# Kernel tuning notes

Hardware: AMD Instinct MI355X
Metric: run time of the kernel (lower is better)

The kernel has to match this reference:

```python
import jax, jax.numpy as jnp
import numpy as np

N = 100000
E = 1600000
IN_C, HID, OUT_C = 512, 256, 32
K = 10
ALPHA = 0.1


def setup_inputs() -> dict:
    key = jax.random.key(0)
    ks = jax.random.split(key, 8)
    x = jax.random.normal(ks[0], (N, IN_C), dtype=jnp.float32)
    edge_index = jax.random.randint(ks[1], (2, E), 0, N, dtype=jnp.int64)
    def lin(k, fan_in, fan_out):
        kw, kb = jax.random.split(k)
        bound = 1.0 / np.sqrt(fan_in)
        W = jax.random.uniform(kw, (fan_out, fan_in), minval=-bound, maxval=bound, dtype=jnp.float32)
        b = jax.random.uniform(kb, (fan_out,), minval=-bound, maxval=bound, dtype=jnp.float32)
        return W, b
    W1, b1 = lin(ks[2], IN_C, HID)
    Wr, br = lin(ks[3], HID, HID)
    W2, b2 = lin(ks[4], HID, OUT_C)
    return {"x": x, "edge_index": edge_index, "W1": W1, "b1": b1,
            "Wr": Wr, "br": br, "W2": W2, "b2": b2}


def _appnp(h0, row, col, norm):
    # h = (1-alpha) * A_hat h + alpha * h0, K steps
    def step(h, _):
        msg = norm[:, None] * h[row]                      # [E+N, C] gather
        agg = jax.ops.segment_sum(msg, col, num_segments=N)
        return (1.0 - ALPHA) * agg + ALPHA * h0, None
    h, _ = jax.lax.scan(step, h0, None, length=K)
    return h


def reference(x, edge_index, W1, b1, Wr, br, W2, b2):
    # eval mode: dropout p=0 -> identity
    h1 = jax.nn.relu(x @ W1.T + b1)
    h2 = jax.nn.relu(h1 @ Wr.T + br)
    x_res = h1 + h2
    h0 = x_res @ W2.T + b2                                # [N, OUT_C]

    # gcn_norm with self-loops (PyG default for APPNP)
    loops = jnp.arange(N, dtype=edge_index.dtype)
    row = jnp.concatenate([edge_index[0], loops])
    col = jnp.concatenate([edge_index[1], loops])
    deg = jax.ops.segment_sum(jnp.ones_like(col, dtype=h0.dtype), col, num_segments=N)
    dinv = jnp.where(deg > 0, jax.lax.rsqrt(deg), 0.0)
    norm = dinv[row] * dinv[col]                          # [E+N]

    return _appnp(h0, row, col, norm)
```

## Files before the change

kernel.cpp:

```cpp
#include <hip/hip_runtime.h>

#define N_NODES 100000
#define E_EDGES 1600000
#define IN_CH   512
#define HID     256
#define OUT_CH  32
#define K_STEPS 10

typedef unsigned short u16;
typedef unsigned int   u32;

typedef __attribute__((ext_vector_type(8))) short bf16x8;
typedef __attribute__((ext_vector_type(4))) float f32x4;

__device__ __forceinline__ float b2f(u16 u) {
    union { u32 i; float f; } x; x.i = ((u32)u) << 16; return x.f;
}
__device__ __forceinline__ u16 f2b(float f) {
    union { float f; u32 u; } x; x.f = f;
    u32 r = x.u + 0x7fffu + ((x.u >> 16) & 1u);
    return (u16)(r >> 16);
}

__device__ __forceinline__ void load_lds16(const void* g, void* l) {
    __builtin_amdgcn_global_load_lds(
        (const __attribute__((address_space(1))) unsigned int*)g,
        (__attribute__((address_space(3))) unsigned int*)l,
        16, 0, 0);
}


__global__ __launch_bounds__(256) void k_cast(const float* __restrict__ in, u16* __restrict__ out, int n4) {
    int i = blockIdx.x * 256 + threadIdx.x;
    if (i < n4) {
        float4 f = ((const float4*)in)[i];
        ushort4 u;
        u.x = f2b(f.x); u.y = f2b(f.y); u.z = f2b(f.z); u.w = f2b(f.w);
        ((ushort4*)out)[i] = u;
    }
}


__global__ __launch_bounds__(256) void k_count(const int* __restrict__ col, int* __restrict__ cnt) {
    int i = blockIdx.x * 256 + threadIdx.x;
    if (i < E_EDGES) atomicAdd(&cnt[col[i]], 1);
}

__global__ __launch_bounds__(256) void k_dinv(const int* __restrict__ cnt, float* __restrict__ dinv) {
    int i = blockIdx.x * 256 + threadIdx.x;
    if (i < N_NODES) dinv[i] = rsqrtf((float)(cnt[i] + 1));
}

__global__ __launch_bounds__(256) void k_blocksum(const int* __restrict__ cnt, int* __restrict__ bs) {
    int b = blockIdx.x, t = threadIdx.x;
    int idx = b * 1024 + t * 4;
    int s = 0;
    #pragma unroll
    for (int j = 0; j < 4; ++j) if (idx + j < N_NODES) s += cnt[idx + j];
    #pragma unroll
    for (int d = 32; d > 0; d >>= 1) s += __shfl_down(s, d, 64);
    __shared__ int smem[4];
    int lane = t & 63, w = t >> 6;
    if (lane == 0) smem[w] = s;
    __syncthreads();
    if (t == 0) bs[b] = smem[0] + smem[1] + smem[2] + smem[3];
}

__global__ void k_scanblocks(const int* __restrict__ bs, int* __restrict__ bo, int nb) {
    int t = threadIdx.x;
    int v = (t < nb) ? bs[t] : 0;
    int incl = v;
    int lane = t & 63, w = t >> 6;
    #pragma unroll
    for (int d = 1; d < 64; d <<= 1) { int tt = __shfl_up(incl, d, 64); if (lane >= d) incl += tt; }
    __shared__ int wsum[2];
    if (lane == 63) wsum[w] = incl;
    __syncthreads();
    int add = (w == 1) ? wsum[0] : 0;
    if (t < nb) bo[t] = add + incl - v;
}

__global__ __launch_bounds__(256) void k_scanwithin(const int* __restrict__ cnt, const int* __restrict__ bo,
                                                    int* __restrict__ off) {
    int b = blockIdx.x, t = threadIdx.x;
    int idx = b * 1024 + t * 4;
    int v[4]; int s = 0;
    #pragma unroll
    for (int j = 0; j < 4; ++j) { v[j] = (idx + j < N_NODES) ? cnt[idx + j] : 0; s += v[j]; }
    int incl = s;
    int lane = t & 63, w = t >> 6;
    #pragma unroll
    for (int d = 1; d < 64; d <<= 1) { int tt = __shfl_up(incl, d, 64); if (lane >= d) incl += tt; }
    __shared__ int wsum[4];
    if (lane == 63) wsum[w] = incl;
    __syncthreads();
    int woff = 0;
    #pragma unroll
    for (int k = 0; k < 4; ++k) if (k < w) woff += wsum[k];
    int run = bo[b] + woff + incl - s;
    #pragma unroll
    for (int j = 0; j < 4; ++j) { if (idx + j < N_NODES) off[idx + j] = run; run += v[j]; }
    if (b == 0 && t == 0) off[N_NODES] = E_EDGES;
}

__global__ __launch_bounds__(256) void k_fill(const int* __restrict__ row, const int* __restrict__ col,
                                              const int* __restrict__ off, int* __restrict__ cursor,
                                              int* __restrict__ csr_row) {
    int i = blockIdx.x * 256 + threadIdx.x;
    if (i < E_EDGES) {
        int c = col[i];
        int pos = off[c] + atomicAdd(&cursor[c], 1);
        csr_row[pos] = row[i];
    }
}


template<int KDIM, bool RESID, bool AF32>
__global__ __launch_bounds__(256) void gemm_mfma(const void* __restrict__ Aptr,
                                                 const u16* __restrict__ Bt,
                                                 const float* __restrict__ bias,
                                                 const u16* __restrict__ resid,
                                                 u16* __restrict__ Out,
                                                 int M) {
    __shared__ u16 As[128 * 32];
    __shared__ u16 Bs[128 * 32];
    const int t = threadIdx.x;
    const int lane = t & 63, w = t >> 6;
    const int row0 = blockIdx.x * 128, col0 = blockIdx.y * 128;

    f32x4 acc[4][4] = {};

    const int rr = lane >> 2;
    const int cc = lane & 3;

    const int wr = (w >> 1) * 64, wc = (w & 1) * 64;
    const int fr = lane & 15, quad = lane >> 4;

    for (int k0 = 0; k0 < KDIM; k0 += 32) {
        if constexpr (AF32) {
            const float* A = (const float*)Aptr;
            #pragma unroll
            for (int it = 0; it < 4; ++it) {
                int chunk = it * 256 + t;
                int row = chunk >> 3, seg = chunk & 7;
                int gr = row0 + row;
                if (gr > M - 1) gr = M - 1;
                float4 f = *(const float4*)&A[(size_t)gr * KDIM + k0 + seg * 4];
                u32 lo = (u32)f2b(f.x) | ((u32)f2b(f.y) << 16);
                u32 hi = (u32)f2b(f.z) | ((u32)f2b(f.w) << 16);
                *(uint2*)&As[row * 32 + seg * 4] = make_uint2(lo, hi);
            }
        } else {
            const u16* A = (const u16*)Aptr;
            #pragma unroll
            for (int rep = 0; rep < 2; ++rep) {
                int ii = w * 2 + rep;
                int gr = row0 + ii * 16 + rr;
                if (gr > M - 1) gr = M - 1;
                load_lds16(A + (size_t)gr * KDIM + k0 + cc * 8, &As[ii * 512]);
            }
        }
        #pragma unroll
        for (int rep = 0; rep < 2; ++rep) {
            int ii = w * 2 + rep;
            int gc = col0 + ii * 16 + rr;
            load_lds16(Bt + (size_t)gc * KDIM + k0 + cc * 8, &Bs[ii * 512]);
        }
        __syncthreads();

        bf16x8 af[4], bfr[4];
        #pragma unroll
        for (int ti = 0; ti < 4; ++ti)
            af[ti] = *(const bf16x8*)&As[(wr + ti * 16 + fr) * 32 + quad * 8];
        #pragma unroll
        for (int tj = 0; tj < 4; ++tj)
            bfr[tj] = *(const bf16x8*)&Bs[(wc + tj * 16 + fr) * 32 + quad * 8];
        #pragma unroll
        for (int ti = 0; ti < 4; ++ti)
            #pragma unroll
            for (int tj = 0; tj < 4; ++tj)
                acc[ti][tj] = __builtin_amdgcn_mfma_f32_16x16x32_bf16(af[ti], bfr[tj], acc[ti][tj], 0, 0, 0);
        __syncthreads();
    }

    #pragma unroll
    for (int tj = 0; tj < 4; ++tj) {
        int col = col0 + wc + tj * 16 + fr;
        float bv = bias[col];
        #pragma unroll
        for (int ti = 0; ti < 4; ++ti) {
            #pragma unroll
            for (int r = 0; r < 4; ++r) {
                int grow = row0 + wr + ti * 16 + quad * 4 + r;
                if (grow < M) {
                    float v = fmaxf(acc[ti][tj][r] + bv, 0.f);
                    if constexpr (RESID) v += b2f(resid[(size_t)grow * HID + col]);
                    Out[(size_t)grow * HID + col] = f2b(v);
                }
            }
        }
    }
}

__global__ __launch_bounds__(256) void gemm_out(const u16* __restrict__ xres, const float* __restrict__ W2,
                                                const float* __restrict__ b2, const float* __restrict__ dinv,
                                                float* __restrict__ h0, u16* __restrict__ p0, int M) {
    constexpr int BM = 128, BK = 16, KDIM = HID;
    __shared__ float As[BK][BM + 4];
    __shared__ float Bs[BK][OUT_CH + 4];
    int t = threadIdx.x;
    int row0 = blockIdx.x * BM;

    float acc[4][4];
    #pragma unroll
    for (int i = 0; i < 4; ++i)
        #pragma unroll
        for (int j = 0; j < 4; ++j) acc[i][j] = 0.f;

    for (int k0 = 0; k0 < KDIM; k0 += BK) {
        #pragma unroll
        for (int rep = 0; rep < 2; ++rep) {
            int idx = rep * 256 + t;
            int r = idx >> 2, ch = idx & 3;
            int gr = row0 + r;
            float v0, v1, v2, v3;
            if (gr < M) {
                ushort4 u = *(const ushort4*)&xres[(size_t)gr * KDIM + k0 + ch * 4];
                v0 = b2f(u.x); v1 = b2f(u.y); v2 = b2f(u.z); v3 = b2f(u.w);
            } else { v0 = v1 = v2 = v3 = 0.f; }
            As[ch * 4 + 0][r] = v0; As[ch * 4 + 1][r] = v1;
            As[ch * 4 + 2][r] = v2; As[ch * 4 + 3][r] = v3;
        }
        if (t < 128) {
            int nn = t >> 2, ch = t & 3;
            float4 f = *(const float4*)&W2[(size_t)nn * KDIM + k0 + ch * 4];
            Bs[ch * 4 + 0][nn] = f.x; Bs[ch * 4 + 1][nn] = f.y;
            Bs[ch * 4 + 2][nn] = f.z; Bs[ch * 4 + 3][nn] = f.w;
        }
        __syncthreads();
        int ty = t >> 3, tx = t & 7;
        #pragma unroll
        for (int kk = 0; kk < BK; ++kk) {
            float a[4], wv[4];
            *(float4*)&a[0] = *(const float4*)&As[kk][ty * 4];
            *(float4*)&wv[0] = *(const float4*)&Bs[kk][tx * 4];
            #pragma unroll
            for (int i = 0; i < 4; ++i)
                #pragma unroll
                for (int j = 0; j < 4; ++j) acc[i][j] = fmaf(a[i], wv[j], acc[i][j]);
        }
        __syncthreads();
    }
    int ty = t >> 3, tx = t & 7;
    #pragma unroll
    for (int i = 0; i < 4; ++i) {
        int gr = row0 + ty * 4 + i;
        if (gr < M) {
            float dv = dinv[gr];
            float4 v;
            v.x = acc[i][0] + b2[tx * 4 + 0];
            v.y = acc[i][1] + b2[tx * 4 + 1];
            v.z = acc[i][2] + b2[tx * 4 + 2];
            v.w = acc[i][3] + b2[tx * 4 + 3];
            *(float4*)&h0[(size_t)gr * OUT_CH + tx * 4] = v;
            ushort4 u;
            u.x = f2b(dv * v.x); u.y = f2b(dv * v.y);
            u.z = f2b(dv * v.z); u.w = f2b(dv * v.w);
            *(ushort4*)&p0[(size_t)gr * OUT_CH + tx * 4] = u;
        }
    }
}


__global__ __launch_bounds__(256) void k_prop(const u32* __restrict__ pin, u32* __restrict__ pout,
                                              float* __restrict__ hout, const float* __restrict__ h0,
                                              const int* __restrict__ off, const int* __restrict__ csr_row,
                                              const float* __restrict__ dinv, int last) {
    int t = threadIdx.x;
    int gw = blockIdx.x * 16 + (t >> 4);
    int l = t & 15;
    int lbase = t & 48;
    int s = off[gw], e = off[gw + 1];
    float dv = dinv[gw];
    u32 selfp = pin[(size_t)gw * 16 + l];
    float2 h0v = ((const float2*)h0)[(size_t)gw * 16 + l];

    float acc0 = 0.f, acc1 = 0.f;
    for (int base = s; base < e; base += 16) {
        int n = e - base; if (n > 16) n = 16;
        int idx = (base + l < e) ? csr_row[base + l] : 0;
        int i = 0;
        for (; i + 3 < n; i += 4) {
            int r0 = __shfl(idx, lbase + i + 0, 64);
            int r1 = __shfl(idx, lbase + i + 1, 64);
            int r2 = __shfl(idx, lbase + i + 2, 64);
            int r3 = __shfl(idx, lbase + i + 3, 64);
            u32 v0 = pin[(size_t)r0 * 16 + l];
            u32 v1 = pin[(size_t)r1 * 16 + l];
            u32 v2 = pin[(size_t)r2 * 16 + l];
            u32 v3 = pin[(size_t)r3 * 16 + l];
            acc0 += (b2f((u16)v0) + b2f((u16)v1)) + (b2f((u16)v2) + b2f((u16)v3));
            acc1 += (b2f((u16)(v0 >> 16)) + b2f((u16)(v1 >> 16))) +
                    (b2f((u16)(v2 >> 16)) + b2f((u16)(v3 >> 16)));
        }
        for (; i < n; ++i) {
            int r = __shfl(idx, lbase + i, 64);
            u32 v = pin[(size_t)r * 16 + l];
            acc0 += b2f((u16)v);
            acc1 += b2f((u16)(v >> 16));
        }
    }
    acc0 += b2f((u16)selfp);
    acc1 += b2f((u16)(selfp >> 16));
    float hc0 = 0.9f * dv * acc0 + 0.1f * h0v.x;
    float hc1 = 0.9f * dv * acc1 + 0.1f * h0v.y;
    if (last) {
        ((float2*)hout)[(size_t)gw * 16 + l] = make_float2(hc0, hc1);
    } else {
        pout[(size_t)gw * 16 + l] = (u32)f2b(dv * hc0) | ((u32)f2b(dv * hc1) << 16);
    }
}


extern "C" void kernel_launch(void* const* d_in, const int* in_sizes, int n_in,
                              void* d_out, int out_size, void* d_ws, size_t ws_size,
                              hipStream_t stream) {
    const float* x  = (const float*)d_in[0];
    const int*   ei = (const int*)d_in[1];
    const float* W1 = (const float*)d_in[2];
    const float* b1 = (const float*)d_in[3];
    const float* Wr = (const float*)d_in[4];
    const float* br = (const float*)d_in[5];
    const float* W2 = (const float*)d_in[6];
    const float* b2 = (const float*)d_in[7];
    float* out = (float*)d_out;

    char* ws = (char*)d_ws;
    size_t off_b = 0;
    auto take = [&](size_t bytes) {
        void* p = ws + off_b;
        off_b += (bytes + 255) & ~(size_t)255;
        return p;
    };

    float* h0      = (float*)take((size_t)N_NODES * OUT_CH * 4);
    u16*   pA      = (u16*)  take((size_t)N_NODES * OUT_CH * 2);
    u16*   pB      = (u16*)  take((size_t)N_NODES * OUT_CH * 2);
    int*   csr_row = (int*)  take((size_t)E_EDGES * 4);
    float* dinv    = (float*)take((size_t)N_NODES * 4);
    int*   cnt     = (int*)  take((size_t)N_NODES * 4);
    int*   offs    = (int*)  take((size_t)(N_NODES + 1) * 4);
    int*   cursor  = (int*)  take((size_t)N_NODES * 4);
    int*   bs      = (int*)  take(1024);
    int*   bo      = (int*)  take(1024);
    u16*   h1      = (u16*)  take((size_t)N_NODES * HID * 2);
    u16*   xres    = (u16*)  take((size_t)N_NODES * HID * 2);
    u16*   W1b     = (u16*)  take((size_t)HID * IN_CH * 2);
    u16*   Wrb     = (u16*)  take((size_t)HID * HID * 2);

    const int* e_row = ei;
    const int* e_col = ei + E_EDGES;

    k_cast<<<(HID * IN_CH / 4 + 255) / 256, 256, 0, stream>>>(W1, W1b, HID * IN_CH / 4);
    k_cast<<<(HID * HID / 4 + 255) / 256, 256, 0, stream>>>(Wr, Wrb, HID * HID / 4);

    dim3 g12((N_NODES + 127) / 128, HID / 128);
    gemm_mfma<IN_CH, false, true><<<g12, 256, 0, stream>>>(x, W1b, b1, nullptr, h1, N_NODES);

    hipMemsetAsync(cnt, 0, (size_t)N_NODES * 4, stream);
    hipMemsetAsync(cursor, 0, (size_t)N_NODES * 4, stream);
    const int NB = (N_NODES + 1023) / 1024;
    k_count<<<(E_EDGES + 255) / 256, 256, 0, stream>>>(e_col, cnt);
    k_dinv<<<(N_NODES + 255) / 256, 256, 0, stream>>>(cnt, dinv);
    k_blocksum<<<NB, 256, 0, stream>>>(cnt, bs);
    k_scanblocks<<<1, 128, 0, stream>>>(bs, bo, NB);
    k_scanwithin<<<NB, 256, 0, stream>>>(cnt, bo, offs);
    k_fill<<<(E_EDGES + 255) / 256, 256, 0, stream>>>(e_row, e_col, offs, cursor, csr_row);

    gemm_mfma<HID, true, false><<<g12, 256, 0, stream>>>(h1, Wrb, br, h1, xres, N_NODES);

    gemm_out<<<(N_NODES + 127) / 128, 256, 0, stream>>>(xres, W2, b2, dinv, h0, pA, N_NODES);

    const u32* pin = (const u32*)pA;
    for (int s = 0; s < K_STEPS; ++s) {
        int last = (s == K_STEPS - 1);
        u32* pout = (u32*)((s & 1) ? pA : pB);
        k_prop<<<N_NODES / 16, 256, 0, stream>>>(pin, pout, out, h0, offs, csr_row, dinv, last);
        pin = pout;
    }
}
```

Before: 919.7 us.

## Pad CSR rows to 16 with a dummy zero node and double-buffer the first GEMM

Each node's CSR segment is rounded up to a multiple of 16 and filled with a dummy index that points at an extra all-zero row in the ping-pong buffers. The propagation kernel can then issue 16 unconditional gathers per chunk with no tail loop or bounds checks, which raises memory-level parallelism. The first GEMM is split into its own kernel that double-buffers LDS and prefetches the fp32 A tile into registers, overlapping global loads with MFMA work. In exchange it adds padded CSR storage, wasted gathers of the zero row, and extra setup kernels and memsets.

Measured after the change: 889.0 us. -3.3%, faster.

```diff
diff --git a/kernel.cpp b/kernel.cpp
--- a/kernel.cpp
+++ b/kernel.cpp
@@ -6,6 +6,7 @@
 #define HID     256
 #define OUT_CH  32
 #define K_STEPS 10
+#define EPAD    (E_EDGES + 16 * N_NODES)
 
 typedef unsigned short u16;
 typedef unsigned int   u32;
@@ -51,12 +52,14 @@
     if (i < N_NODES) dinv[i] = rsqrtf((float)(cnt[i] + 1));
 }
 
+__device__ __forceinline__ int pad16(int v) { return (v + 15) & ~15; }
+
 __global__ __launch_bounds__(256) void k_blocksum(const int* __restrict__ cnt, int* __restrict__ bs) {
     int b = blockIdx.x, t = threadIdx.x;
     int idx = b * 1024 + t * 4;
     int s = 0;
     #pragma unroll
-    for (int j = 0; j < 4; ++j) if (idx + j < N_NODES) s += cnt[idx + j];
+    for (int j = 0; j < 4; ++j) if (idx + j < N_NODES) s += pad16(cnt[idx + j]);
     #pragma unroll
     for (int d = 32; d > 0; d >>= 1) s += __shfl_down(s, d, 64);
     __shared__ int smem[4];
@@ -86,7 +89,7 @@
     int idx = b * 1024 + t * 4;
     int v[4]; int s = 0;
     #pragma unroll
-    for (int j = 0; j < 4; ++j) { v[j] = (idx + j < N_NODES) ? cnt[idx + j] : 0; s += v[j]; }
+    for (int j = 0; j < 4; ++j) { v[j] = (idx + j < N_NODES) ? pad16(cnt[idx + j]) : 0; s += v[j]; }
     int incl = s;
     int lane = t & 63, w = t >> 6;
     #pragma unroll
@@ -100,7 +103,16 @@
     int run = bo[b] + woff + incl - s;
     #pragma unroll
     for (int j = 0; j < 4; ++j) { if (idx + j < N_NODES) off[idx + j] = run; run += v[j]; }
-    if (b == 0 && t == 0) off[N_NODES] = E_EDGES;
+}
+
+__global__ __launch_bounds__(256) void k_total(const int* __restrict__ bo, const int* __restrict__ bs,
+                                               int* __restrict__ off, int nb) {
+    off[N_NODES] = bo[nb - 1] + bs[nb - 1];
+}
+
+__global__ __launch_bounds__(256) void k_filldummy(int* __restrict__ csr_row) {
+    int i = blockIdx.x * 256 + threadIdx.x;
+    if (i < EPAD) csr_row[i] = N_NODES;
 }
 
 __global__ __launch_bounds__(256) void k_fill(const int* __restrict__ row, const int* __restrict__ col,
@@ -115,8 +127,101 @@
 }
 
 
-template<int KDIM, bool RESID, bool AF32>
-__global__ __launch_bounds__(256) void gemm_mfma(const void* __restrict__ Aptr,
+__global__ __launch_bounds__(256) void gemm1_mfma(const float* __restrict__ A,
+                                                  const u16* __restrict__ Bt,
+                                                  const float* __restrict__ bias,
+                                                  u16* __restrict__ Out, int M) {
+    __shared__ u16 As[2][128 * 32];
+    __shared__ u16 Bs[2][128 * 32];
+    const int t = threadIdx.x;
+    const int lane = t & 63, w = t >> 6;
+    const int row0 = blockIdx.x * 128, col0 = blockIdx.y * 128;
+    const int rr = lane >> 2, cc = lane & 3;
+    const int wr = (w >> 1) * 64, wc = (w & 1) * 64;
+    const int fr = lane & 15, quad = lane >> 4;
+
+    f32x4 acc[4][4] = {};
+    float4 fp[4];
+    int arow[4], aseg[4];
+    #pragma unroll
+    for (int it = 0; it < 4; ++it) {
+        int chunk = it * 256 + t;
+        arow[it] = chunk >> 3; aseg[it] = chunk & 7;
+    }
+
+    auto prefA = [&](int k0) {
+        #pragma unroll
+        for (int it = 0; it < 4; ++it) {
+            int gr = row0 + arow[it]; if (gr > M - 1) gr = M - 1;
+            fp[it] = *(const float4*)&A[(size_t)gr * IN_CH + k0 + aseg[it] * 4];
+        }
+    };
+    auto writeA = [&](int b) {
+        #pragma unroll
+        for (int it = 0; it < 4; ++it) {
+            u32 lo = (u32)f2b(fp[it].x) | ((u32)f2b(fp[it].y) << 16);
+            u32 hi = (u32)f2b(fp[it].z) | ((u32)f2b(fp[it].w) << 16);
+            *(uint2*)&As[b][arow[it] * 32 + aseg[it] * 4] = make_uint2(lo, hi);
+        }
+    };
+    auto loadB = [&](int k0, int b) {
+        #pragma unroll
+        for (int rep = 0; rep < 2; ++rep) {
+            int ii = w * 2 + rep;
+            int gc = col0 + ii * 16 + rr;
+            load_lds16(Bt + (size_t)gc * IN_CH + k0 + cc * 8, &Bs[b][ii * 512]);
+        }
+    };
+
+    prefA(0);
+    loadB(0, 0);
+    writeA(0);
+    __syncthreads();
+
+    for (int it = 0; it < IN_CH / 32; ++it) {
+        const int cur = it & 1;
+        const bool more = (it < IN_CH / 32 - 1);
+        if (more) prefA((it + 1) * 32);
+        bf16x8 af[4], bfr[4];
+        #pragma unroll
+        for (int ti = 0; ti < 4; ++ti)
+            af[ti] = *(const bf16x8*)&As[cur][(wr + ti * 16 + fr) * 32 + quad * 8];
+        #pragma unroll
+        for (int tj = 0; tj < 4; ++tj)
+            bfr[tj] = *(const bf16x8*)&Bs[cur][(wc + tj * 16 + fr) * 32 + quad * 8];
+        #pragma unroll
+        for (int ti = 0; ti < 4; ++ti)
+            #pragma unroll
+            for (int tj = 0; tj < 4; ++tj)
+                acc[ti][tj] = __builtin_amdgcn_mfma_f32_16x16x32_bf16(af[ti], bfr[tj], acc[ti][tj], 0, 0, 0);
+        if (more) {
+            loadB((it + 1) * 32, cur ^ 1);
+            writeA(cur ^ 1);
+            __syncthreads();
+        }
+    }
+
+    #pragma unroll
+    for (int tj = 0; tj < 4; ++tj) {
+        int col = col0 + wc + tj * 16 + fr;
+        float bv = bias[col];
+        #pragma unroll
+        for (int ti = 0; ti < 4; ++ti) {
+            #pragma unroll
+            for (int r = 0; r < 4; ++r) {
+                int grow = row0 + wr + ti * 16 + quad * 4 + r;
+                if (grow < M) {
+                    float v = fmaxf(acc[ti][tj][r] + bv, 0.f);
+                    Out[(size_t)grow * HID + col] = f2b(v);
+                }
+            }
+        }
+    }
+}
+
+
+template<int KDIM, bool RESID>
+__global__ __launch_bounds__(256) void gemm_mfma(const u16* __restrict__ A,
                                                  const u16* __restrict__ Bt,
                                                  const float* __restrict__ bias,
                                                  const u16* __restrict__ resid,
@@ -129,36 +234,17 @@
     const int row0 = blockIdx.x * 128, col0 = blockIdx.y * 128;
 
     f32x4 acc[4][4] = {};
-
-    const int rr = lane >> 2;
-    const int cc = lane & 3;
-
+    const int rr = lane >> 2, cc = lane & 3;
     const int wr = (w >> 1) * 64, wc = (w & 1) * 64;
     const int fr = lane & 15, quad = lane >> 4;
 
     for (int k0 = 0; k0 < KDIM; k0 += 32) {
-        if constexpr (AF32) {
-            const float* A = (const float*)Aptr;
-            #pragma unroll
-            for (int it = 0; it < 4; ++it) {
-                int chunk = it * 256 + t;
-                int row = chunk >> 3, seg = chunk & 7;
-                int gr = row0 + row;
-                if (gr > M - 1) gr = M - 1;
-                float4 f = *(const float4*)&A[(size_t)gr * KDIM + k0 + seg * 4];
-                u32 lo = (u32)f2b(f.x) | ((u32)f2b(f.y) << 16);
-                u32 hi = (u32)f2b(f.z) | ((u32)f2b(f.w) << 16);
-                *(uint2*)&As[row * 32 + seg * 4] = make_uint2(lo, hi);
-            }
-        } else {
-            const u16* A = (const u16*)Aptr;
-            #pragma unroll
-            for (int rep = 0; rep < 2; ++rep) {
-                int ii = w * 2 + rep;
-                int gr = row0 + ii * 16 + rr;
-                if (gr > M - 1) gr = M - 1;
-                load_lds16(A + (size_t)gr * KDIM + k0 + cc * 8, &As[ii * 512]);
-            }
+        #pragma unroll
+        for (int rep = 0; rep < 2; ++rep) {
+            int ii = w * 2 + rep;
+            int gr = row0 + ii * 16 + rr;
+            if (gr > M - 1) gr = M - 1;
+            load_lds16(A + (size_t)gr * KDIM + k0 + cc * 8, &As[ii * 512]);
         }
         #pragma unroll
         for (int rep = 0; rep < 2; ++rep) {
@@ -287,27 +373,18 @@
 
     float acc0 = 0.f, acc1 = 0.f;
     for (int base = s; base < e; base += 16) {
-        int n = e - base; if (n > 16) n = 16;
-        int idx = (base + l < e) ? csr_row[base + l] : 0;
-        int i = 0;
-        for (; i + 3 < n; i += 4) {
-            int r0 = __shfl(idx, lbase + i + 0, 64);
-            int r1 = __shfl(idx, lbase + i + 1, 64);
-            int r2 = __shfl(idx, lbase + i + 2, 64);
-            int r3 = __shfl(idx, lbase + i + 3, 64);
-            u32 v0 = pin[(size_t)r0 * 16 + l];
-            u32 v1 = pin[(size_t)r1 * 16 + l];
-            u32 v2 = pin[(size_t)r2 * 16 + l];
-            u32 v3 = pin[(size_t)r3 * 16 + l];
-            acc0 += (b2f((u16)v0) + b2f((u16)v1)) + (b2f((u16)v2) + b2f((u16)v3));
-            acc1 += (b2f((u16)(v0 >> 16)) + b2f((u16)(v1 >> 16))) +
-                    (b2f((u16)(v2 >> 16)) + b2f((u16)(v3 >> 16)));
-        }
-        for (; i < n; ++i) {
+        int idx = csr_row[base + l];
+        u32 v[16];
+        #pragma unroll
+        for (int i = 0; i < 16; ++i) {
             int r = __shfl(idx, lbase + i, 64);
-            u32 v = pin[(size_t)r * 16 + l];
-            acc0 += b2f((u16)v);
-            acc1 += b2f((u16)(v >> 16));
+            v[i] = pin[(size_t)r * 16 + l];
+        }
+        #pragma unroll
+        for (int i = 0; i < 16; ++i) {
+            union { u32 u; float f; } a, b;
+            a.u = v[i] << 16; b.u = v[i] & 0xffff0000u;
+            acc0 += a.f; acc1 += b.f;
         }
     }
     acc0 += b2f((u16)selfp);
@@ -344,9 +421,9 @@
     };
 
     float* h0      = (float*)take((size_t)N_NODES * OUT_CH * 4);
-    u16*   pA      = (u16*)  take((size_t)N_NODES * OUT_CH * 2);
-    u16*   pB      = (u16*)  take((size_t)N_NODES * OUT_CH * 2);
-    int*   csr_row = (int*)  take((size_t)E_EDGES * 4);
+    u16*   pA      = (u16*)  take((size_t)(N_NODES + 1) * OUT_CH * 2);
+    u16*   pB      = (u16*)  take((size_t)(N_NODES + 1) * OUT_CH * 2);
+    int*   csr_row = (int*)  take((size_t)EPAD * 4);
     float* dinv    = (float*)take((size_t)N_NODES * 4);
     int*   cnt     = (int*)  take((size_t)N_NODES * 4);
     int*   offs    = (int*)  take((size_t)(N_NODES + 1) * 4);
@@ -365,19 +442,23 @@
     k_cast<<<(HID * HID / 4 + 255) / 256, 256, 0, stream>>>(Wr, Wrb, HID * HID / 4);
 
     dim3 g12((N_NODES + 127) / 128, HID / 128);
-    gemm_mfma<IN_CH, false, true><<<g12, 256, 0, stream>>>(x, W1b, b1, nullptr, h1, N_NODES);
+    gemm1_mfma<<<g12, 256, 0, stream>>>(x, W1b, b1, h1, N_NODES);
 
     hipMemsetAsync(cnt, 0, (size_t)N_NODES * 4, stream);
     hipMemsetAsync(cursor, 0, (size_t)N_NODES * 4, stream);
+    hipMemsetAsync(pA + (size_t)N_NODES * OUT_CH, 0, OUT_CH * 2, stream);
+    hipMemsetAsync(pB + (size_t)N_NODES * OUT_CH, 0, OUT_CH * 2, stream);
     const int NB = (N_NODES + 1023) / 1024;
     k_count<<<(E_EDGES + 255) / 256, 256, 0, stream>>>(e_col, cnt);
     k_dinv<<<(N_NODES + 255) / 256, 256, 0, stream>>>(cnt, dinv);
     k_blocksum<<<NB, 256, 0, stream>>>(cnt, bs);
     k_scanblocks<<<1, 128, 0, stream>>>(bs, bo, NB);
     k_scanwithin<<<NB, 256, 0, stream>>>(cnt, bo, offs);
+    k_total<<<1, 1, 0, stream>>>(bo, bs, offs, NB);
+    k_filldummy<<<(EPAD + 255) / 256, 256, 0, stream>>>(csr_row);
     k_fill<<<(E_EDGES + 255) / 256, 256, 0, stream>>>(e_row, e_col, offs, cursor, csr_row);
 
-    gemm_mfma<HID, true, false><<<g12, 256, 0, stream>>>(h1, Wrb, br, h1, xres, N_NODES);
+    gemm_mfma<HID, true><<<g12, 256, 0, stream>>>(h1, Wrb, br, h1, xres, N_NODES);
 
     gemm_out<<<(N_NODES + 127) / 128, 256, 0, stream>>>(xres, W2, b2, dinv, h0, pA, N_NODES);
 
```
